# Optimization experiments

Measured on AMD Instinct MI355X. Metric: run time of the kernel, lower is better.

## Reference

```python
import jax, jax.numpy as jnp
import numpy as np

I = 512  # input_size
H = 512  # hidden_size
L = 512  # sequence length
N = 64   # batch


def setup_inputs() -> dict:
    key = jax.random.key(0)
    ks = jax.random.split(key, 12)
    s_ih = 1.0 / np.sqrt(H)
    inp = {
        "input": jax.random.normal(ks[0], (L, N, I), dtype=jnp.float32),
        "h_0": jax.random.normal(ks[1], (2, N, H), dtype=jnp.float32),
        # layer 0 params
        "W_ih_l0": jax.random.uniform(ks[2], (H, I), jnp.float32, -s_ih, s_ih),
        "W_hh_l0": jax.random.uniform(ks[3], (H, H), jnp.float32, -s_ih, s_ih),
        "b_ih_l0": jax.random.uniform(ks[4], (H,), jnp.float32, -s_ih, s_ih),
        "b_hh_l0": jax.random.uniform(ks[5], (H,), jnp.float32, -s_ih, s_ih),
        # layer 1 params (input is layer 0 hidden state, size H)
        "W_ih_l1": jax.random.uniform(ks[6], (H, H), jnp.float32, -s_ih, s_ih),
        "W_hh_l1": jax.random.uniform(ks[7], (H, H), jnp.float32, -s_ih, s_ih),
        "b_ih_l1": jax.random.uniform(ks[8], (H,), jnp.float32, -s_ih, s_ih),
        "b_hh_l1": jax.random.uniform(ks[9], (H,), jnp.float32, -s_ih, s_ih),
    }
    return inp


def reference(input, h_0, W_ih_l0, W_hh_l0, b_ih_l0, b_hh_l0,
              W_ih_l1, W_hh_l1, b_ih_l1, b_hh_l1):
    """2-layer Elman RNN with tanh: h[t] = tanh(x[t] W_ih^T + b_ih + h[t-1] W_hh^T + b_hh).
    Layer 1 consumes layer 0's hidden state at the same timestep.
    Returns (output: (L, N, H), h_n: (2, N, H)).
    """

    def step(carry, x_t):
        h0, h1 = carry  # each (N, H)
        h0_new = jnp.tanh(x_t @ W_ih_l0.T + b_ih_l0 + h0 @ W_hh_l0.T + b_hh_l0)
        h1_new = jnp.tanh(h0_new @ W_ih_l1.T + b_ih_l1 + h1 @ W_hh_l1.T + b_hh_l1)
        return (h0_new, h1_new), h1_new

    (h0_n, h1_n), output = jax.lax.scan(step, (h_0[0], h_0[1]), input)
    h_n = jnp.stack([h0_n, h1_n], axis=0)
    return output, h_n
```

## Files before the change

kernel.cpp:

```cpp
#include <hip/hip_runtime.h>
#include <hip/hip_bf16.h>
#include <math.h>

#define L_SEQ 512
#define N_B   64
#define H_D   512
#define M_TOT (L_SEQ * N_B)

typedef unsigned short u16;
typedef unsigned long long u64;
typedef __attribute__((ext_vector_type(8))) short short8;
typedef __attribute__((ext_vector_type(4))) float f32x4;
typedef __attribute__((ext_vector_type(4))) int i32x4;
typedef __attribute__((ext_vector_type(2))) int i32x2;

__device__ __forceinline__ u16 f2bf(float f) {
    unsigned int u = __builtin_bit_cast(unsigned int, f);
    u = u + 0x7fffu + ((u >> 16) & 1u);
    return (u16)(u >> 16);
}

__device__ __forceinline__ float fast_tanh(float x) {
    float e = __expf(2.0f * x);
    return 1.0f - 2.0f / (e + 1.0f);
}

__device__ __forceinline__ void st_h(u16* p, u16 v) {
    __hip_atomic_store(p, v, __ATOMIC_RELAXED, __HIP_MEMORY_SCOPE_AGENT);
}
__device__ __forceinline__ void st_flag(int* p, int v) {
    __hip_atomic_store(p, v, __ATOMIC_RELAXED, __HIP_MEMORY_SCOPE_AGENT);
}

#define FSTRIDE 16

#define LD16(f, p)                                                          \
  asm volatile(                                                             \
    "global_load_dwordx4 %0, %16, off\n\t"                                  \
    "global_load_dwordx4 %1, %16, off offset:64\n\t"                        \
    "global_load_dwordx4 %2, %16, off offset:128\n\t"                       \
    "global_load_dwordx4 %3, %16, off offset:192\n\t"                       \
    "global_load_dwordx4 %4, %16, off offset:256\n\t"                       \
    "global_load_dwordx4 %5, %16, off offset:320\n\t"                       \
    "global_load_dwordx4 %6, %16, off offset:384\n\t"                       \
    "global_load_dwordx4 %7, %16, off offset:448\n\t"                       \
    "global_load_dwordx4 %8, %16, off offset:512\n\t"                       \
    "global_load_dwordx4 %9, %16, off offset:576\n\t"                       \
    "global_load_dwordx4 %10, %16, off offset:640\n\t"                      \
    "global_load_dwordx4 %11, %16, off offset:704\n\t"                      \
    "global_load_dwordx4 %12, %16, off offset:768\n\t"                      \
    "global_load_dwordx4 %13, %16, off offset:832\n\t"                      \
    "global_load_dwordx4 %14, %16, off offset:896\n\t"                      \
    "global_load_dwordx4 %15, %16, off offset:960\n\t"                      \
    "s_waitcnt vmcnt(0)"                                                    \
    : "=&v"(f[0]), "=&v"(f[1]), "=&v"(f[2]), "=&v"(f[3]),                   \
      "=&v"(f[4]), "=&v"(f[5]), "=&v"(f[6]), "=&v"(f[7]),                   \
      "=&v"(f[8]), "=&v"(f[9]), "=&v"(f[10]), "=&v"(f[11]),                 \
      "=&v"(f[12]), "=&v"(f[13]), "=&v"(f[14]), "=&v"(f[15])                \
    : "v"(p) : "memory")

#define LD16X2(f, g, p0, p1)                                                \
  asm volatile(                                                             \
    "global_load_dwordx4 %0, %32, off\n\t"                                  \
    "global_load_dwordx4 %16, %33, off\n\t"                                 \
    "global_load_dwordx4 %1, %32, off offset:64\n\t"                        \
    "global_load_dwordx4 %17, %33, off offset:64\n\t"                       \
    "global_load_dwordx4 %2, %32, off offset:128\n\t"                       \
    "global_load_dwordx4 %18, %33, off offset:128\n\t"                      \
    "global_load_dwordx4 %3, %32, off offset:192\n\t"                       \
    "global_load_dwordx4 %19, %33, off offset:192\n\t"                      \
    "global_load_dwordx4 %4, %32, off offset:256\n\t"                       \
    "global_load_dwordx4 %20, %33, off offset:256\n\t"                      \
    "global_load_dwordx4 %5, %32, off offset:320\n\t"                       \
    "global_load_dwordx4 %21, %33, off offset:320\n\t"                      \
    "global_load_dwordx4 %6, %32, off offset:384\n\t"                       \
    "global_load_dwordx4 %22, %33, off offset:384\n\t"                      \
    "global_load_dwordx4 %7, %32, off offset:448\n\t"                       \
    "global_load_dwordx4 %23, %33, off offset:448\n\t"                      \
    "global_load_dwordx4 %8, %32, off offset:512\n\t"                       \
    "global_load_dwordx4 %24, %33, off offset:512\n\t"                      \
    "global_load_dwordx4 %9, %32, off offset:576\n\t"                       \
    "global_load_dwordx4 %25, %33, off offset:576\n\t"                      \
    "global_load_dwordx4 %10, %32, off offset:640\n\t"                      \
    "global_load_dwordx4 %26, %33, off offset:640\n\t"                      \
    "global_load_dwordx4 %11, %32, off offset:704\n\t"                      \
    "global_load_dwordx4 %27, %33, off offset:704\n\t"                      \
    "global_load_dwordx4 %12, %32, off offset:768\n\t"                      \
    "global_load_dwordx4 %28, %33, off offset:768\n\t"                      \
    "global_load_dwordx4 %13, %32, off offset:832\n\t"                      \
    "global_load_dwordx4 %29, %33, off offset:832\n\t"                      \
    "global_load_dwordx4 %14, %32, off offset:896\n\t"                      \
    "global_load_dwordx4 %30, %33, off offset:896\n\t"                      \
    "global_load_dwordx4 %15, %32, off offset:960\n\t"                      \
    "global_load_dwordx4 %31, %33, off offset:960\n\t"                      \
    "s_waitcnt vmcnt(0)"                                                    \
    : "=&v"(f[0]), "=&v"(f[1]), "=&v"(f[2]), "=&v"(f[3]),                   \
      "=&v"(f[4]), "=&v"(f[5]), "=&v"(f[6]), "=&v"(f[7]),                   \
      "=&v"(f[8]), "=&v"(f[9]), "=&v"(f[10]), "=&v"(f[11]),                 \
      "=&v"(f[12]), "=&v"(f[13]), "=&v"(f[14]), "=&v"(f[15]),               \
      "=&v"(g[0]), "=&v"(g[1]), "=&v"(g[2]), "=&v"(g[3]),                   \
      "=&v"(g[4]), "=&v"(g[5]), "=&v"(g[6]), "=&v"(g[7]),                   \
      "=&v"(g[8]), "=&v"(g[9]), "=&v"(g[10]), "=&v"(g[11]),                 \
      "=&v"(g[12]), "=&v"(g[13]), "=&v"(g[14]), "=&v"(g[15])                \
    : "v"(p0), "v"(p1) : "memory")

#define WAITVM asm volatile("s_waitcnt vmcnt(0)" ::: "memory")

__device__ __host__ __forceinline__ int perm32(int j) {
    return (((j >> 3) & 3) << 2) | (j & 3) | (((j >> 2) & 1) << 4);
}

__global__ void k_prep(const float* __restrict__ x,
                       const float* __restrict__ w0ih, const float* __restrict__ w0hh,
                       const float* __restrict__ b0i,  const float* __restrict__ b0h,
                       const float* __restrict__ w1ih, const float* __restrict__ w1hh,
                       const float* __restrict__ b1i,  const float* __restrict__ b1h,
                       u16* __restrict__ xb,
                       u16* __restrict__ w0ihb, u16* __restrict__ w0hhb,
                       u16* __restrict__ w1ihb, u16* __restrict__ w1hhb,
                       float* __restrict__ bias0, float* __restrict__ bias1,
                       int* __restrict__ flags)
{
    const int stride = gridDim.x * blockDim.x;
    const int tid = blockIdx.x * blockDim.x + threadIdx.x;
    for (int i = tid; i < M_TOT * H_D / 4; i += stride) {
        const float4 v = ((const float4*)x)[i];
        ushort4 o;
        o.x = f2bf(v.x); o.y = f2bf(v.y); o.z = f2bf(v.z); o.w = f2bf(v.w);
        ((ushort4*)xb)[i] = o;
    }
    for (int i = tid; i < H_D * H_D; i += stride) {
        const int p  = i & (H_D - 1);
        const int pc = (i & ~(H_D - 1)) | (p & ~31) | perm32(p & 31);
        w0ihb[i] = f2bf(w0ih[i]);
        w0hhb[i] = f2bf(w0hh[pc]);
        w1ihb[i] = f2bf(w1ih[pc]);
        w1hhb[i] = f2bf(w1hh[i]);
    }
    if (tid < H_D) {
        bias0[tid] = b0i[tid] + b0h[tid];
        bias1[tid] = b1i[tid] + b1h[tid];
    }
    if (tid < 48 * FSTRIDE) flags[tid] = 0;
}

__global__ __launch_bounds__(256)
void k_gemm(const u16* __restrict__ A, const u16* __restrict__ W,
            const float* __restrict__ bias, float* __restrict__ out)
{
    __shared__ u16 As[128][40];
    __shared__ u16 Ws[128][40];
    const int m0 = blockIdx.x * 128;
    const int n0 = blockIdx.y * 128;
    const int tid = threadIdx.x;
    const int w = tid >> 6, l = tid & 63, q = l >> 4, lr = l & 15;
    const int mw = (w >> 1) * 64, nw = (w & 1) * 64;
    const int skg = (tid & 3) * 8;
    const int smr = tid >> 2;

    f32x4 acc[4][4];
    #pragma unroll
    for (int i = 0; i < 4; ++i)
        #pragma unroll
        for (int j = 0; j < 4; ++j)
            acc[i][j] = (f32x4){0.f, 0.f, 0.f, 0.f};

    for (int kk = 0; kk < H_D; kk += 32) {
        *(uint4*)&As[smr][skg]      = *(const uint4*)(A + (size_t)(m0 + smr) * H_D + kk + skg);
        *(uint4*)&As[smr + 64][skg] = *(const uint4*)(A + (size_t)(m0 + smr + 64) * H_D + kk + skg);
        *(uint4*)&Ws[smr][skg]      = *(const uint4*)(W + (size_t)(n0 + smr) * H_D + kk + skg);
        *(uint4*)&Ws[smr + 64][skg] = *(const uint4*)(W + (size_t)(n0 + smr + 64) * H_D + kk + skg);
        __syncthreads();
        short8 af[4], bf[4];
        #pragma unroll
        for (int rt = 0; rt < 4; ++rt) af[rt] = *(const short8*)&As[mw + rt*16 + lr][q*8];
        #pragma unroll
        for (int nt = 0; nt < 4; ++nt) bf[nt] = *(const short8*)&Ws[nw + nt*16 + lr][q*8];
        #pragma unroll
        for (int rt = 0; rt < 4; ++rt)
            #pragma unroll
            for (int nt = 0; nt < 4; ++nt)
                acc[rt][nt] = __builtin_amdgcn_mfma_f32_16x16x32_bf16(af[rt], bf[nt], acc[rt][nt], 0, 0, 0);
        __syncthreads();
    }
    #pragma unroll
    for (int nt = 0; nt < 4; ++nt) {
        const int col = n0 + nw + nt*16 + lr;
        const float bv = bias[col];
        #pragma unroll
        for (int rt = 0; rt < 4; ++rt) {
            #pragma unroll
            for (int r = 0; r < 4; ++r) {
                const int row = m0 + mw + rt*16 + q*4 + r;
                out[(size_t)row * H_D + col] = acc[rt][nt][r] + bv;
            }
        }
    }
}

__global__ __launch_bounds__(256, 1)
void k_rec_fused(const u16* __restrict__ Whh0, const u16* __restrict__ Wih1,
                 const u16* __restrict__ Whh1,
                 const float* __restrict__ h_init,
                 const float* __restrict__ pre0,
                 const float* __restrict__ bias1,
                 u16* __restrict__ h0buf, u16* __restrict__ h1buf,
                 float* __restrict__ out, float* __restrict__ hn,
                 int* __restrict__ flags0, int* __restrict__ flags1)
{
    (void)__hip_atomic_load(flags0, __ATOMIC_ACQUIRE, __HIP_MEMORY_SCOPE_AGENT);

    const int tid = threadIdx.x;
    const int w = tid >> 6, l = tid & 63, q = l >> 4, lr = l & 15;
    const int r0 = w * 16;
    const int m = r0 + lr;

    if (blockIdx.x < 16) {
        const int c = blockIdx.x;
        const int nbase = c * 32;
        short8 breg[16][2];
        #pragma unroll
        for (int kt = 0; kt < 16; ++kt)
            #pragma unroll
            for (int nt = 0; nt < 2; ++nt)
                breg[kt][nt] = *(const short8*)(Whh0 + (size_t)(nbase + nt*16 + lr) * H_D + kt*32 + q*8);

        #pragma unroll
        for (int j = 0; j < 8; ++j) {
            int idx = l * 8 + j;
            int row = r0 + (idx >> 5);
            int pos = idx & 31;
            st_h(h0buf + (size_t)row * H_D + nbase + pos,
                 f2bf(h_init[row * H_D + nbase + perm32(pos)]));
        }
        WAITVM;
        __syncthreads();
        if (tid == 0) st_flag(flags0 + c * FSTRIDE, 1);

        for (int t = 0; t < L_SEQ; ++t) {
            const float* pt = pre0 + (size_t)t * (N_B * H_D)
                            + (size_t)(r0 + lr) * H_D + nbase + q*4;
            f32x4 acc0a = *(const f32x4*)pt;
            f32x4 acc1a = *(const f32x4*)(pt + 16);
            f32x4 acc0b = (f32x4){0.f,0.f,0.f,0.f};
            f32x4 acc1b = (f32x4){0.f,0.f,0.f,0.f};
            f32x4 acc0c = (f32x4){0.f,0.f,0.f,0.f};
            f32x4 acc1c = (f32x4){0.f,0.f,0.f,0.f};
            f32x4 acc0d = (f32x4){0.f,0.f,0.f,0.f};
            f32x4 acc1d = (f32x4){0.f,0.f,0.f,0.f};

            if (w == 0) {
                const int* p = flags0 + (l & 15) * FSTRIDE;
                while (true) {
                    int v = __hip_atomic_load(p, __ATOMIC_RELAXED, __HIP_MEMORY_SCOPE_AGENT);
                    if (__all(v >= t + 1)) break;
                }
                asm volatile("" ::: "memory");
            }
            __syncthreads();

            const u16* hs = h0buf + ((size_t)t * N_B + m) * H_D + q*8;
            i32x4 f[16];
            LD16(f, hs);
            #pragma unroll
            for (int kt = 0; kt < 16; kt += 4) {
                acc0a = __builtin_amdgcn_mfma_f32_16x16x32_bf16(breg[kt][0],   __builtin_bit_cast(short8, f[kt]),   acc0a, 0, 0, 0);
                acc1a = __builtin_amdgcn_mfma_f32_16x16x32_bf16(breg[kt][1],   __builtin_bit_cast(short8, f[kt]),   acc1a, 0, 0, 0);
                acc0b = __builtin_amdgcn_mfma_f32_16x16x32_bf16(breg[kt+1][0], __builtin_bit_cast(short8, f[kt+1]), acc0b, 0, 0, 0);
                acc1b = __builtin_amdgcn_mfma_f32_16x16x32_bf16(breg[kt+1][1], __builtin_bit_cast(short8, f[kt+1]), acc1b, 0, 0, 0);
                acc0c = __builtin_amdgcn_mfma_f32_16x16x32_bf16(breg[kt+2][0], __builtin_bit_cast(short8, f[kt+2]), acc0c, 0, 0, 0);
                acc1c = __builtin_amdgcn_mfma_f32_16x16x32_bf16(breg[kt+2][1], __builtin_bit_cast(short8, f[kt+2]), acc1c, 0, 0, 0);
                acc0d = __builtin_amdgcn_mfma_f32_16x16x32_bf16(breg[kt+3][0], __builtin_bit_cast(short8, f[kt+3]), acc0d, 0, 0, 0);
                acc1d = __builtin_amdgcn_mfma_f32_16x16x32_bf16(breg[kt+3][1], __builtin_bit_cast(short8, f[kt+3]), acc1d, 0, 0, 0);
            }
            float v0[4], v1[4];
            #pragma unroll
            for (int r = 0; r < 4; ++r) {
                v0[r] = fast_tanh((acc0a[r] + acc0b[r]) + (acc0c[r] + acc0d[r]));
                v1[r] = fast_tanh((acc1a[r] + acc1b[r]) + (acc1c[r] + acc1d[r]));
            }
            i32x4 dd;
            dd[0] = (int)((unsigned)f2bf(v0[0]) | ((unsigned)f2bf(v0[1]) << 16));
            dd[1] = (int)((unsigned)f2bf(v0[2]) | ((unsigned)f2bf(v0[3]) << 16));
            dd[2] = (int)((unsigned)f2bf(v1[0]) | ((unsigned)f2bf(v1[1]) << 16));
            dd[3] = (int)((unsigned)f2bf(v1[2]) | ((unsigned)f2bf(v1[3]) << 16));
            u16* hd = h0buf + (size_t)(t+1) * (N_B * H_D)
                    + (size_t)(r0 + lr) * H_D + nbase + q*8;
            asm volatile(
                "global_store_dwordx4 %1, %0, off sc1"
                :: "v"(dd), "v"(hd) : "memory");
            WAITVM;
            __syncthreads();
            if (tid == 0) st_flag(flags0 + c * FSTRIDE, t + 2);

            if (t == L_SEQ - 1) {
                f32x4 o0 = {v0[0], v0[1], v0[2], v0[3]};
                f32x4 o1 = {v1[0], v1[1], v1[2], v1[3]};
                *(f32x4*)(hn + (size_t)(r0 + lr) * H_D + nbase + q*4)      = o0;
                *(f32x4*)(hn + (size_t)(r0 + lr) * H_D + nbase + 16 + q*4) = o1;
            }
        }
    } else {
        const int c = blockIdx.x - 16;
        const int nbase = c * 16;
        short8 bregI[16], bregH[16];
        #pragma unroll
        for (int kt = 0; kt < 16; ++kt) {
            bregI[kt] = *(const short8*)(Wih1 + (size_t)(nbase + lr) * H_D + kt*32 + q*8);
            bregH[kt] = *(const short8*)(Whh1 + (size_t)(nbase + lr) * H_D + kt*32 + q*8);
        }
        const f32x4 bv4 = *(const f32x4*)(bias1 + nbase + q*4);

        const float* hi1 = h_init + N_B * H_D;
        #pragma unroll
        for (int j = 0; j < 4; ++j) {
            int idx = l * 4 + j;
            int row = r0 + (idx >> 4);
            int col = nbase + (idx & 15);
            st_h(h1buf + (size_t)row * H_D + col, f2bf(hi1[row * H_D + col]));
        }
        WAITVM;
        __syncthreads();
        if (tid == 0) st_flag(flags1 + c * FSTRIDE, 1);

        for (int t = 0; t < L_SEQ; ++t) {
            if (w == 0) {
                const int* p;
                int need;
                if (l < 16)      { p = flags0 + l * FSTRIDE;        need = t + 2; }
                else if (l < 48) { p = flags1 + (l - 16) * FSTRIDE; need = t + 1; }
                else             { p = flags0;                      need = 0;     }
                while (true) {
                    int v = __hip_atomic_load(p, __ATOMIC_RELAXED, __HIP_MEMORY_SCOPE_AGENT);
                    if (__all(v >= need)) break;
                }
                asm volatile("" ::: "memory");
            }
            __syncthreads();

            const u16* p0 = h0buf + ((size_t)(t+1) * N_B + m) * H_D + q*8;
            const u16* p1 = h1buf + ((size_t)t     * N_B + m) * H_D + q*8;
            i32x4 f[16], g[16];
            LD16X2(f, g, p0, p1);
            f32x4 accA = bv4;
            f32x4 accB = (f32x4){0.f,0.f,0.f,0.f};
            f32x4 accC = (f32x4){0.f,0.f,0.f,0.f};
            f32x4 accD = (f32x4){0.f,0.f,0.f,0.f};
            #pragma unroll
            for (int kt = 0; kt < 16; kt += 2) {
                accA = __builtin_amdgcn_mfma_f32_16x16x32_bf16(bregI[kt],   __builtin_bit_cast(short8, f[kt]),   accA, 0, 0, 0);
                accB = __builtin_amdgcn_mfma_f32_16x16x32_bf16(bregH[kt],   __builtin_bit_cast(short8, g[kt]),   accB, 0, 0, 0);
                accC = __builtin_amdgcn_mfma_f32_16x16x32_bf16(bregI[kt+1], __builtin_bit_cast(short8, f[kt+1]), accC, 0, 0, 0);
                accD = __builtin_amdgcn_mfma_f32_16x16x32_bf16(bregH[kt+1], __builtin_bit_cast(short8, g[kt+1]), accD, 0, 0, 0);
            }
            float v[4];
            #pragma unroll
            for (int r = 0; r < 4; ++r)
                v[r] = fast_tanh((accA[r] + accB[r]) + (accC[r] + accD[r]));
            i32x2 d;
            d[0] = (int)((unsigned)f2bf(v[0]) | ((unsigned)f2bf(v[1]) << 16));
            d[1] = (int)((unsigned)f2bf(v[2]) | ((unsigned)f2bf(v[3]) << 16));
            u16* hd = h1buf + (size_t)(t+1) * (N_B * H_D)
                    + (size_t)(r0 + lr) * H_D + nbase + q*4;
            asm volatile(
                "global_store_dwordx2 %1, %0, off sc1"
                :: "v"(d), "v"(hd) : "memory");
            WAITVM;
            __syncthreads();
            if (tid == 0) st_flag(flags1 + c * FSTRIDE, t + 2);

            f32x4 ov = {v[0], v[1], v[2], v[3]};
            *(f32x4*)(out + (size_t)t * (N_B * H_D)
                      + (size_t)(r0 + lr) * H_D + nbase + q*4) = ov;
            if (t == L_SEQ - 1)
                *(f32x4*)(hn + (size_t)(N_B + r0 + lr) * H_D + nbase + q*4) = ov;
        }
    }
}

extern "C" void kernel_launch(void* const* d_in, const int* in_sizes, int n_in,
                              void* d_out, int out_size, void* d_ws, size_t ws_size,
                              hipStream_t stream)
{
    (void)in_sizes; (void)n_in; (void)out_size; (void)ws_size;
    const float* x    = (const float*)d_in[0];
    const float* h0   = (const float*)d_in[1];
    const float* w0ih = (const float*)d_in[2];
    const float* w0hh = (const float*)d_in[3];
    const float* b0i  = (const float*)d_in[4];
    const float* b0h  = (const float*)d_in[5];
    const float* w1ih = (const float*)d_in[6];
    const float* w1hh = (const float*)d_in[7];
    const float* b1i  = (const float*)d_in[8];
    const float* b1h  = (const float*)d_in[9];
    float* out = (float*)d_out;
    float* hn  = out + (size_t)M_TOT * H_D;

    char* ws = (char*)d_ws;
    size_t off = 0;
    u16* w0ihb = (u16*)(ws + off);   off += (size_t)H_D * H_D * 2;
    u16* w0hhb = (u16*)(ws + off);   off += (size_t)H_D * H_D * 2;
    u16* w1ihb = (u16*)(ws + off);   off += (size_t)H_D * H_D * 2;
    u16* w1hhb = (u16*)(ws + off);   off += (size_t)H_D * H_D * 2;
    float* bias0 = (float*)(ws + off); off += H_D * 4;
    float* bias1 = (float*)(ws + off); off += H_D * 4;
    int* flags   = (int*)(ws + off);   off += 48 * FSTRIDE * 4;
    int* flags0  = flags;
    int* flags1  = flags + 16 * FSTRIDE;
    u16* h0buf   = (u16*)(ws + off);   off += (size_t)(L_SEQ + 1) * N_B * H_D * 2;
    float* pre0  = (float*)(ws + off); off += (size_t)M_TOT * H_D * 4;
    u16* h1buf   = (u16*)(ws + off);   off += (size_t)(L_SEQ + 1) * N_B * H_D * 2;
    u16* xb      = h1buf;

    k_prep<<<2048, 256, 0, stream>>>(x, w0ih, w0hh, b0i, b0h, w1ih, w1hh, b1i, b1h,
                                     xb, w0ihb, w0hhb, w1ihb, w1hhb,
                                     bias0, bias1, flags);
    k_gemm<<<dim3(M_TOT/128, H_D/128), 256, 0, stream>>>(xb, w0ihb, bias0, pre0);
    k_rec_fused<<<48, 256, 0, stream>>>(w0hhb, w1ihb, w1hhb, h0, pre0, bias1,
                                        h0buf, h1buf, out, hn, flags0, flags1);
}
```

Measured before the change: 2.935 ms.

## Replace flag-based inter-block sync with sentinel-poll data loads

Removes the per-step flag counters, the store waits, the __syncthreads and the flag spin loops. Consumers now poll the hidden-state buffers directly, reloading until no dword equals a canonical-NaN sentinel pattern. A new k_init kernel pre-fills both h buffers with that sentinel. This takes a flag round-trip and two block barriers off the serial critical path of every timestep. In exchange it adds a memset-like pass over about 67MB and relies on per-dword visibility of stores, and on bf16 pairs never legitimately being 0x7FC0 (tanh outputs cannot be NaN).

```diff
diff --git a/kernel.cpp b/kernel.cpp
--- a/kernel.cpp
+++ b/kernel.cpp
@@ -6,6 +6,8 @@
 #define N_B   64
 #define H_D   512
 #define M_TOT (L_SEQ * N_B)
+
+#define CANI ((int)0x7FC07FC0)
 
 typedef unsigned short u16;
 typedef unsigned long long u64;
@@ -25,33 +27,24 @@
     return 1.0f - 2.0f / (e + 1.0f);
 }
 
-__device__ __forceinline__ void st_h(u16* p, u16 v) {
-    __hip_atomic_store(p, v, __ATOMIC_RELAXED, __HIP_MEMORY_SCOPE_AGENT);
-}
-__device__ __forceinline__ void st_flag(int* p, int v) {
-    __hip_atomic_store(p, v, __ATOMIC_RELAXED, __HIP_MEMORY_SCOPE_AGENT);
-}
-
-#define FSTRIDE 16
-
-#define LD16(f, p)                                                          \
+#define LD16P(f, p)                                                         \
   asm volatile(                                                             \
-    "global_load_dwordx4 %0, %16, off\n\t"                                  \
-    "global_load_dwordx4 %1, %16, off offset:64\n\t"                        \
-    "global_load_dwordx4 %2, %16, off offset:128\n\t"                       \
-    "global_load_dwordx4 %3, %16, off offset:192\n\t"                       \
-    "global_load_dwordx4 %4, %16, off offset:256\n\t"                       \
-    "global_load_dwordx4 %5, %16, off offset:320\n\t"                       \
-    "global_load_dwordx4 %6, %16, off offset:384\n\t"                       \
-    "global_load_dwordx4 %7, %16, off offset:448\n\t"                       \
-    "global_load_dwordx4 %8, %16, off offset:512\n\t"                       \
-    "global_load_dwordx4 %9, %16, off offset:576\n\t"                       \
-    "global_load_dwordx4 %10, %16, off offset:640\n\t"                      \
-    "global_load_dwordx4 %11, %16, off offset:704\n\t"                      \
-    "global_load_dwordx4 %12, %16, off offset:768\n\t"                      \
-    "global_load_dwordx4 %13, %16, off offset:832\n\t"                      \
-    "global_load_dwordx4 %14, %16, off offset:896\n\t"                      \
-    "global_load_dwordx4 %15, %16, off offset:960\n\t"                      \
+    "global_load_dwordx4 %0, %16, off sc1\n\t"                              \
+    "global_load_dwordx4 %1, %16, off offset:64 sc1\n\t"                    \
+    "global_load_dwordx4 %2, %16, off offset:128 sc1\n\t"                   \
+    "global_load_dwordx4 %3, %16, off offset:192 sc1\n\t"                   \
+    "global_load_dwordx4 %4, %16, off offset:256 sc1\n\t"                   \
+    "global_load_dwordx4 %5, %16, off offset:320 sc1\n\t"                   \
+    "global_load_dwordx4 %6, %16, off offset:384 sc1\n\t"                   \
+    "global_load_dwordx4 %7, %16, off offset:448 sc1\n\t"                   \
+    "global_load_dwordx4 %8, %16, off offset:512 sc1\n\t"                   \
+    "global_load_dwordx4 %9, %16, off offset:576 sc1\n\t"                   \
+    "global_load_dwordx4 %10, %16, off offset:640 sc1\n\t"                  \
+    "global_load_dwordx4 %11, %16, off offset:704 sc1\n\t"                  \
+    "global_load_dwordx4 %12, %16, off offset:768 sc1\n\t"                  \
+    "global_load_dwordx4 %13, %16, off offset:832 sc1\n\t"                  \
+    "global_load_dwordx4 %14, %16, off offset:896 sc1\n\t"                  \
+    "global_load_dwordx4 %15, %16, off offset:960 sc1\n\t"                  \
     "s_waitcnt vmcnt(0)"                                                    \
     : "=&v"(f[0]), "=&v"(f[1]), "=&v"(f[2]), "=&v"(f[3]),                   \
       "=&v"(f[4]), "=&v"(f[5]), "=&v"(f[6]), "=&v"(f[7]),                   \
@@ -59,40 +52,40 @@
       "=&v"(f[12]), "=&v"(f[13]), "=&v"(f[14]), "=&v"(f[15])                \
     : "v"(p) : "memory")
 
-#define LD16X2(f, g, p0, p1)                                                \
+#define LD16X2P(f, g, p0, p1)                                               \
   asm volatile(                                                             \
-    "global_load_dwordx4 %0, %32, off\n\t"                                  \
-    "global_load_dwordx4 %16, %33, off\n\t"                                 \
-    "global_load_dwordx4 %1, %32, off offset:64\n\t"                        \
-    "global_load_dwordx4 %17, %33, off offset:64\n\t"                       \
-    "global_load_dwordx4 %2, %32, off offset:128\n\t"                       \
-    "global_load_dwordx4 %18, %33, off offset:128\n\t"                      \
-    "global_load_dwordx4 %3, %32, off offset:192\n\t"                       \
-    "global_load_dwordx4 %19, %33, off offset:192\n\t"                      \
-    "global_load_dwordx4 %4, %32, off offset:256\n\t"                       \
-    "global_load_dwordx4 %20, %33, off offset:256\n\t"                      \
-    "global_load_dwordx4 %5, %32, off offset:320\n\t"                       \
-    "global_load_dwordx4 %21, %33, off offset:320\n\t"                      \
-    "global_load_dwordx4 %6, %32, off offset:384\n\t"                       \
-    "global_load_dwordx4 %22, %33, off offset:384\n\t"                      \
-    "global_load_dwordx4 %7, %32, off offset:448\n\t"                       \
-    "global_load_dwordx4 %23, %33, off offset:448\n\t"                      \
-    "global_load_dwordx4 %8, %32, off offset:512\n\t"                       \
-    "global_load_dwordx4 %24, %33, off offset:512\n\t"                      \
-    "global_load_dwordx4 %9, %32, off offset:576\n\t"                       \
-    "global_load_dwordx4 %25, %33, off offset:576\n\t"                      \
-    "global_load_dwordx4 %10, %32, off offset:640\n\t"                      \
-    "global_load_dwordx4 %26, %33, off offset:640\n\t"                      \
-    "global_load_dwordx4 %11, %32, off offset:704\n\t"                      \
-    "global_load_dwordx4 %27, %33, off offset:704\n\t"                      \
-    "global_load_dwordx4 %12, %32, off offset:768\n\t"                      \
-    "global_load_dwordx4 %28, %33, off offset:768\n\t"                      \
-    "global_load_dwordx4 %13, %32, off offset:832\n\t"                      \
-    "global_load_dwordx4 %29, %33, off offset:832\n\t"                      \
-    "global_load_dwordx4 %14, %32, off offset:896\n\t"                      \
-    "global_load_dwordx4 %30, %33, off offset:896\n\t"                      \
-    "global_load_dwordx4 %15, %32, off offset:960\n\t"                      \
-    "global_load_dwordx4 %31, %33, off offset:960\n\t"                      \
+    "global_load_dwordx4 %0, %32, off sc1\n\t"                              \
+    "global_load_dwordx4 %16, %33, off sc1\n\t"                             \
+    "global_load_dwordx4 %1, %32, off offset:64 sc1\n\t"                    \
+    "global_load_dwordx4 %17, %33, off offset:64 sc1\n\t"                   \
+    "global_load_dwordx4 %2, %32, off offset:128 sc1\n\t"                   \
+    "global_load_dwordx4 %18, %33, off offset:128 sc1\n\t"                  \
+    "global_load_dwordx4 %3, %32, off offset:192 sc1\n\t"                   \
+    "global_load_dwordx4 %19, %33, off offset:192 sc1\n\t"                  \
+    "global_load_dwordx4 %4, %32, off offset:256 sc1\n\t"                   \
+    "global_load_dwordx4 %20, %33, off offset:256 sc1\n\t"                  \
+    "global_load_dwordx4 %5, %32, off offset:320 sc1\n\t"                   \
+    "global_load_dwordx4 %21, %33, off offset:320 sc1\n\t"                  \
+    "global_load_dwordx4 %6, %32, off offset:384 sc1\n\t"                   \
+    "global_load_dwordx4 %22, %33, off offset:384 sc1\n\t"                  \
+    "global_load_dwordx4 %7, %32, off offset:448 sc1\n\t"                   \
+    "global_load_dwordx4 %23, %33, off offset:448 sc1\n\t"                  \
+    "global_load_dwordx4 %8, %32, off offset:512 sc1\n\t"                   \
+    "global_load_dwordx4 %24, %33, off offset:512 sc1\n\t"                  \
+    "global_load_dwordx4 %9, %32, off offset:576 sc1\n\t"                   \
+    "global_load_dwordx4 %25, %33, off offset:576 sc1\n\t"                  \
+    "global_load_dwordx4 %10, %32, off offset:640 sc1\n\t"                  \
+    "global_load_dwordx4 %26, %33, off offset:640 sc1\n\t"                  \
+    "global_load_dwordx4 %11, %32, off offset:704 sc1\n\t"                  \
+    "global_load_dwordx4 %27, %33, off offset:704 sc1\n\t"                  \
+    "global_load_dwordx4 %12, %32, off offset:768 sc1\n\t"                  \
+    "global_load_dwordx4 %28, %33, off offset:768 sc1\n\t"                  \
+    "global_load_dwordx4 %13, %32, off offset:832 sc1\n\t"                  \
+    "global_load_dwordx4 %29, %33, off offset:832 sc1\n\t"                  \
+    "global_load_dwordx4 %14, %32, off offset:896 sc1\n\t"                  \
+    "global_load_dwordx4 %30, %33, off offset:896 sc1\n\t"                  \
+    "global_load_dwordx4 %15, %32, off offset:960 sc1\n\t"                  \
+    "global_load_dwordx4 %31, %33, off offset:960 sc1\n\t"                  \
     "s_waitcnt vmcnt(0)"                                                    \
     : "=&v"(f[0]), "=&v"(f[1]), "=&v"(f[2]), "=&v"(f[3]),                   \
       "=&v"(f[4]), "=&v"(f[5]), "=&v"(f[6]), "=&v"(f[7]),                   \
@@ -104,7 +97,7 @@
       "=&v"(g[12]), "=&v"(g[13]), "=&v"(g[14]), "=&v"(g[15])                \
     : "v"(p0), "v"(p1) : "memory")
 
-#define WAITVM asm volatile("s_waitcnt vmcnt(0)" ::: "memory")
+#define SEGOK(v) (((v)[0] != CANI) & ((v)[1] != CANI) & ((v)[2] != CANI) & ((v)[3] != CANI))
 
 __device__ __host__ __forceinline__ int perm32(int j) {
     return (((j >> 3) & 3) << 2) | (j & 3) | (((j >> 2) & 1) << 4);
@@ -118,8 +111,7 @@
                        u16* __restrict__ xb,
                        u16* __restrict__ w0ihb, u16* __restrict__ w0hhb,
                        u16* __restrict__ w1ihb, u16* __restrict__ w1hhb,
-                       float* __restrict__ bias0, float* __restrict__ bias1,
-                       int* __restrict__ flags)
+                       float* __restrict__ bias0, float* __restrict__ bias1)
 {
     const int stride = gridDim.x * blockDim.x;
     const int tid = blockIdx.x * blockDim.x + threadIdx.x;
@@ -141,7 +133,16 @@
         bias0[tid] = b0i[tid] + b0h[tid];
         bias1[tid] = b1i[tid] + b1h[tid];
     }
-    if (tid < 48 * FSTRIDE) flags[tid] = 0;
+}
+
+__global__ void k_init(i32x4* __restrict__ h0c, i32x4* __restrict__ h1c, int n16)
+{
+    const int stride = gridDim.x * blockDim.x;
+    const i32x4 c = {CANI, CANI, CANI, CANI};
+    for (int i = blockIdx.x * blockDim.x + threadIdx.x; i < n16; i += stride) {
+        h0c[i] = c;
+        h1c[i] = c;
+    }
 }
 
 __global__ __launch_bounds__(256)
@@ -205,10 +206,9 @@
                  const float* __restrict__ pre0,
                  const float* __restrict__ bias1,
                  u16* __restrict__ h0buf, u16* __restrict__ h1buf,
-                 float* __restrict__ out, float* __restrict__ hn,
-                 int* __restrict__ flags0, int* __restrict__ flags1)
+                 float* __restrict__ out, float* __restrict__ hn)
 {
-    (void)__hip_atomic_load(flags0, __ATOMIC_ACQUIRE, __HIP_MEMORY_SCOPE_AGENT);
+    (void)__hip_atomic_load((const int*)h0buf, __ATOMIC_ACQUIRE, __HIP_MEMORY_SCOPE_AGENT);
 
     const int tid = threadIdx.x;
     const int w = tid >> 6, l = tid & 63, q = l >> 4, lr = l & 15;
@@ -226,16 +226,17 @@
                 breg[kt][nt] = *(const short8*)(Whh0 + (size_t)(nbase + nt*16 + lr) * H_D + kt*32 + q*8);
 
         #pragma unroll
-        for (int j = 0; j < 8; ++j) {
-            int idx = l * 8 + j;
+        for (int j = 0; j < 4; ++j) {
+            int idx = l * 8 + j * 2;
             int row = r0 + (idx >> 5);
             int pos = idx & 31;
-            st_h(h0buf + (size_t)row * H_D + nbase + pos,
-                 f2bf(h_init[row * H_D + nbase + perm32(pos)]));
-        }
-        WAITVM;
-        __syncthreads();
-        if (tid == 0) st_flag(flags0 + c * FSTRIDE, 1);
+            unsigned lo = f2bf(h_init[row * H_D + nbase + perm32(pos)]);
+            unsigned hi = f2bf(h_init[row * H_D + nbase + perm32(pos + 1)]);
+            unsigned dv = lo | (hi << 16);
+            u16* dp = h0buf + (size_t)row * H_D + nbase + pos;
+            asm volatile("global_store_dword %0, %1, off sc1"
+                         :: "v"(dp), "v"(dv) : "memory");
+        }
 
         for (int t = 0; t < L_SEQ; ++t) {
             const float* pt = pre0 + (size_t)t * (N_B * H_D)
@@ -249,19 +250,16 @@
             f32x4 acc0d = (f32x4){0.f,0.f,0.f,0.f};
             f32x4 acc1d = (f32x4){0.f,0.f,0.f,0.f};
 
-            if (w == 0) {
-                const int* p = flags0 + (l & 15) * FSTRIDE;
-                while (true) {
-                    int v = __hip_atomic_load(p, __ATOMIC_RELAXED, __HIP_MEMORY_SCOPE_AGENT);
-                    if (__all(v >= t + 1)) break;
-                }
-                asm volatile("" ::: "memory");
-            }
-            __syncthreads();
-
             const u16* hs = h0buf + ((size_t)t * N_B + m) * H_D + q*8;
             i32x4 f[16];
-            LD16(f, hs);
+            while (true) {
+                LD16P(f, hs);
+                int ok = 1;
+                #pragma unroll
+                for (int i = 0; i < 16; ++i) ok &= SEGOK(f[i]);
+                if (__all(ok)) break;
+            }
+
             #pragma unroll
             for (int kt = 0; kt < 16; kt += 4) {
                 acc0a = __builtin_amdgcn_mfma_f32_16x16x32_bf16(breg[kt][0],   __builtin_bit_cast(short8, f[kt]),   acc0a, 0, 0, 0);
@@ -289,9 +287,6 @@
             asm volatile(
                 "global_store_dwordx4 %1, %0, off sc1"
                 :: "v"(dd), "v"(hd) : "memory");
-            WAITVM;
-            __syncthreads();
-            if (tid == 0) st_flag(flags0 + c * FSTRIDE, t + 2);
 
             if (t == L_SEQ - 1) {
                 f32x4 o0 = {v0[0], v0[1], v0[2], v0[3]};
@@ -313,35 +308,29 @@
 
         const float* hi1 = h_init + N_B * H_D;
         #pragma unroll
-        for (int j = 0; j < 4; ++j) {
-            int idx = l * 4 + j;
+        for (int j = 0; j < 2; ++j) {
+            int idx = l * 4 + j * 2;
             int row = r0 + (idx >> 4);
             int col = nbase + (idx & 15);
-            st_h(h1buf + (size_t)row * H_D + col, f2bf(hi1[row * H_D + col]));
-        }
-        WAITVM;
-        __syncthreads();
-        if (tid == 0) st_flag(flags1 + c * FSTRIDE, 1);
+            unsigned lo = f2bf(hi1[row * H_D + col]);
+            unsigned hi = f2bf(hi1[row * H_D + col + 1]);
+            unsigned dv = lo | (hi << 16);
+            u16* dp = h1buf + (size_t)row * H_D + col;
+            asm volatile("global_store_dword %0, %1, off sc1"
+                         :: "v"(dp), "v"(dv) : "memory");
+        }
 
         for (int t = 0; t < L_SEQ; ++t) {
-            if (w == 0) {
-                const int* p;
-                int need;
-                if (l < 16)      { p = flags0 + l * FSTRIDE;        need = t + 2; }
-                else if (l < 48) { p = flags1 + (l - 16) * FSTRIDE; need = t + 1; }
-                else             { p = flags0;                      need = 0;     }
-                while (true) {
-                    int v = __hip_atomic_load(p, __ATOMIC_RELAXED, __HIP_MEMORY_SCOPE_AGENT);
-                    if (__all(v >= need)) break;
-                }
-                asm volatile("" ::: "memory");
-            }
-            __syncthreads();
-
             const u16* p0 = h0buf + ((size_t)(t+1) * N_B + m) * H_D + q*8;
             const u16* p1 = h1buf + ((size_t)t     * N_B + m) * H_D + q*8;
             i32x4 f[16], g[16];
-            LD16X2(f, g, p0, p1);
+            while (true) {
+                LD16X2P(f, g, p0, p1);
+                int ok = 1;
+                #pragma unroll
+                for (int i = 0; i < 16; ++i) ok &= SEGOK(f[i]) & SEGOK(g[i]);
+                if (__all(ok)) break;
+            }
             f32x4 accA = bv4;
             f32x4 accB = (f32x4){0.f,0.f,0.f,0.f};
             f32x4 accC = (f32x4){0.f,0.f,0.f,0.f};
@@ -365,9 +354,6 @@
             asm volatile(
                 "global_store_dwordx2 %1, %0, off sc1"
                 :: "v"(d), "v"(hd) : "memory");
-            WAITVM;
-            __syncthreads();
-            if (tid == 0) st_flag(flags1 + c * FSTRIDE, t + 2);
 
             f32x4 ov = {v[0], v[1], v[2], v[3]};
             *(f32x4*)(out + (size_t)t * (N_B * H_D)
@@ -404,18 +390,18 @@
     u16* w1hhb = (u16*)(ws + off);   off += (size_t)H_D * H_D * 2;
     float* bias0 = (float*)(ws + off); off += H_D * 4;
     float* bias1 = (float*)(ws + off); off += H_D * 4;
-    int* flags   = (int*)(ws + off);   off += 48 * FSTRIDE * 4;
-    int* flags0  = flags;
-    int* flags1  = flags + 16 * FSTRIDE;
     u16* h0buf   = (u16*)(ws + off);   off += (size_t)(L_SEQ + 1) * N_B * H_D * 2;
     float* pre0  = (float*)(ws + off); off += (size_t)M_TOT * H_D * 4;
     u16* h1buf   = (u16*)(ws + off);   off += (size_t)(L_SEQ + 1) * N_B * H_D * 2;
     u16* xb      = h1buf;
 
+    const int n16 = (L_SEQ + 1) * N_B * H_D * 2 / 16;
+
     k_prep<<<2048, 256, 0, stream>>>(x, w0ih, w0hh, b0i, b0h, w1ih, w1hh, b1i, b1h,
                                      xb, w0ihb, w0hhb, w1ihb, w1hhb,
-                                     bias0, bias1, flags);
+                                     bias0, bias1);
     k_gemm<<<dim3(M_TOT/128, H_D/128), 256, 0, stream>>>(xb, w0ihb, bias0, pre0);
+    k_init<<<2048, 256, 0, stream>>>((i32x4*)h0buf, (i32x4*)h1buf, n16);
     k_rec_fused<<<48, 256, 0, stream>>>(w0hhb, w1ihb, w1hhb, h0, pre0, bias1,
-                                        h0buf, h1buf, out, hn, flags0, flags1);
-}
+                                        h0buf, h1buf, out, hn);
+}
```

Result: slower. 3.879 ms (+32.1%).
